# Kernel tuning notes

Measured on AMD Instinct MI355X. Metric: run time of the kernel, lower is better.

Reference implementation:

```python
import jax, jax.numpy as jnp
import numpy as np

EMBED_DIM = 512
NUM_HEADS = 8
HEAD_DIM = EMBED_DIM // NUM_HEADS


def setup_inputs() -> dict:
    key = jax.random.key(0)
    k_x, k_qkv, k_proj, k_pb = jax.random.split(key, 4)
    B, N, C = 2, 4096, EMBED_DIM
    x = jax.random.normal(k_x, (B, N, C), dtype=jnp.float32)
    # nn.Linear(embed_dim, 3*embed_dim, bias=False): weight [3C, C], y = x @ W.T
    s = 1.0 / np.sqrt(C)
    w_qkv = jax.random.uniform(k_qkv, (3 * C, C), dtype=jnp.float32, minval=-s, maxval=s)
    w_proj = jax.random.uniform(k_proj, (C, C), dtype=jnp.float32, minval=-s, maxval=s)
    b_proj = jax.random.uniform(k_pb, (C,), dtype=jnp.float32, minval=-s, maxval=s)
    return {"x": x, "w_qkv": w_qkv, "w_proj": w_proj, "b_proj": b_proj}


def reference(x, w_qkv, w_proj, b_proj):
    B, N, C = x.shape
    H, D = NUM_HEADS, HEAD_DIM
    scale = D ** -0.5
    qkv = jnp.einsum('bnc,fc->bnf', x, w_qkv)           # [B, N, 3C]
    qkv = qkv.reshape(B, N, 3, H, D)
    q, k, v = [jnp.transpose(qkv[:, :, i], (0, 2, 1, 3)) for i in range(3)]  # [B,H,N,D]
    attn = jnp.einsum('bhnd,bhmd->bhnm', q, k) * scale  # [B,H,N,N]
    # additive causal mask: -inf above the diagonal
    causal = jnp.triu(jnp.full((N, N), -jnp.inf, dtype=attn.dtype), k=1)
    attn = jax.nn.softmax(attn + causal, axis=-1)
    out = jnp.einsum('bhnm,bhmd->bhnd', attn, v)        # [B,H,N,D]
    out = jnp.transpose(out, (0, 2, 1, 3)).reshape(B, N, C)
    return jnp.einsum('bnc,oc->bno', out, w_proj) + b_proj
```

## Files before the change

### kernel.cpp

```cpp
#include <hip/hip_runtime.h>
#include <hip/hip_bf16.h>


typedef __attribute__((ext_vector_type(8))) short s16x8;
typedef __attribute__((ext_vector_type(4))) float f32x4;

#define QSCALE 0.18033688011112042f

__device__ __forceinline__ ushort f2bf(float f) {
  unsigned u = __float_as_uint(f);
  u = (u + 0x7FFFu + ((u >> 16) & 1u)) >> 16;
  return (ushort)u;
}

__device__ __forceinline__ unsigned cvt_pk_bf16(float a, float b) {
  unsigned r;
  asm("v_cvt_pk_bf16_f32 %0, %1, %2" : "=v"(r) : "v"(a), "v"(b));
  return r;
}

__device__ __forceinline__ float bflo(unsigned u) { return __uint_as_float(u << 16); }
__device__ __forceinline__ float bfhi(unsigned u) { return __uint_as_float(u & 0xffff0000u); }

__global__ __launch_bounds__(256) void cvt_all(const float* __restrict__ x,
                                               const float* __restrict__ wq,
                                               const float* __restrict__ wp,
                                               ushort* __restrict__ xb,
                                               ushort* __restrict__ wqb,
                                               ushort* __restrict__ wpb) {
  int i = blockIdx.x * 256 + threadIdx.x;
  const float* src;
  ushort* dst;
  int off;
  if (i < 1048576) {
    src = x; dst = xb; off = i;
  } else if (i < 1245184) {
    src = wq; dst = wqb; off = i - 1048576;
  } else {
    src = wp; dst = wpb; off = i - 1245184;
  }
  float4 v = reinterpret_cast<const float4*>(src)[off];
  ushort4 o;
  o.x = f2bf(v.x); o.y = f2bf(v.y); o.z = f2bf(v.z); o.w = f2bf(v.w);
  reinterpret_cast<ushort4*>(dst)[off] = o;
}

template <int EPI>
__global__ __launch_bounds__(256) void gemm_bt(const ushort* __restrict__ A,
                                               const ushort* __restrict__ W,
                                               ushort* __restrict__ q_ws,
                                               ushort* __restrict__ k_ws,
                                               ushort* __restrict__ vt_ws,
                                               float* __restrict__ outf,
                                               const float* __restrict__ bias) {
  __shared__ ushort As[2][128 * 32];
  __shared__ ushort Bs[2][128 * 32];
  const int tid = threadIdx.x;
  const int lane = tid & 63, wv = tid >> 6;
  const int wm = wv >> 1, wn = wv & 1;
  const int l15 = lane & 15, g = lane >> 4;
  const int tm = blockIdx.y * 128, tn = blockIdx.x * 128;

  f32x4 acc[4][4] = {};

#define GSTAGE(BUF, K0)                                                                    \
  do {                                                                                     \
    _Pragma("unroll") for (int it = 0; it < 2; ++it) {                                     \
      int slot = it * 256 + tid;                                                           \
      int row = slot >> 2;                                                                 \
      int ch = (slot & 3) ^ ((row >> 1) & 3);                                              \
      const int sb = (it * 256 + wv * 64) * 8;        \
      __builtin_amdgcn_global_load_lds(                                                    \
          (const __attribute__((address_space(1))) void*)(A + (size_t)(tm + row) * 512 +   \
                                                          (K0) + ch * 8),                  \
          (__attribute__((address_space(3))) void*)(&As[BUF][0] + sb), 16, 0, 0);          \
      __builtin_amdgcn_global_load_lds(                                                    \
          (const __attribute__((address_space(1))) void*)(W + (size_t)(tn + row) * 512 +   \
                                                          (K0) + ch * 8),                  \
          (__attribute__((address_space(3))) void*)(&Bs[BUF][0] + sb), 16, 0, 0);          \
    }                                                                                      \
  } while (0)

  GSTAGE(0, 0);
  __syncthreads();
  int cur = 0;
  for (int t = 0; t < 16; ++t) {
    if (t < 15) GSTAGE(cur ^ 1, (t + 1) * 32);
    s16x8 af[4], bfr[4];
#pragma unroll
    for (int i = 0; i < 4; ++i) {
      int Ra = wm * 64 + i * 16 + l15;
      af[i] = reinterpret_cast<const s16x8*>(&As[cur][0])[Ra * 4 + (g ^ ((Ra >> 1) & 3))];
      int Rb = wn * 64 + i * 16 + l15;
      bfr[i] = reinterpret_cast<const s16x8*>(&Bs[cur][0])[Rb * 4 + (g ^ ((Rb >> 1) & 3))];
    }
#pragma unroll
    for (int mi = 0; mi < 4; ++mi)
#pragma unroll
      for (int ni = 0; ni < 4; ++ni)
        acc[mi][ni] =
            __builtin_amdgcn_mfma_f32_16x16x32_bf16(af[mi], bfr[ni], acc[mi][ni], 0, 0, 0);
    __syncthreads();
    cur ^= 1;
  }
#undef GSTAGE

  const int rowb = tm + wm * 64 + g * 4;
  const int colb = tn + wn * 64 + l15;
#pragma unroll
  for (int mi = 0; mi < 4; ++mi) {
#pragma unroll
    for (int ni = 0; ni < 4; ++ni) {
      int r0 = rowb + mi * 16;
      int col = colb + ni * 16;
      if (EPI == 0) {
        int i3 = col >> 9, h = (col >> 6) & 7, d = col & 63;
        int b = r0 >> 12;
        int bh = b * 8 + h;
        if (i3 == 2) {
          int n0 = r0 & 4095;
          int kt = n0 >> 6, ce = (n0 >> 5) & 1, ge = (n0 >> 3) & 3, je = n0 & 7;
          int nbe = d >> 4, le = d & 15;
          ushort4 pk;
          pk.x = f2bf(acc[mi][ni][0]);
          pk.y = f2bf(acc[mi][ni][1]);
          pk.z = f2bf(acc[mi][ni][2]);
          pk.w = f2bf(acc[mi][ni][3]);
          *reinterpret_cast<ushort4*>(
              vt_ws + (((size_t)bh * 64 + kt) * 8 + nbe * 2 + ce) * 512 + (ge * 16 + le) * 8 +
              je) = pk;
        } else if (i3 == 1) {
          int ce = d >> 5, ge = (d >> 3) & 3, je = d & 7;
#pragma unroll
          for (int r = 0; r < 4; ++r) {
            int n = (r0 + r) & 4095;
            int kt = n >> 6, le = n & 15, nbe = (n >> 4) & 3;
            k_ws[(((size_t)bh * 64 + kt) * 8 + nbe * 2 + ce) * 512 + (ge * 16 + le) * 8 + je] =
                f2bf(acc[mi][ni][r]);
          }
        } else {
          int n0 = r0 & 4095;
#pragma unroll
          for (int r = 0; r < 4; ++r)
            q_ws[((size_t)bh * 4096 + (n0 + r)) * 64 + d] = f2bf(acc[mi][ni][r] * QSCALE);
        }
      } else {
#pragma unroll
        for (int r = 0; r < 4; ++r)
          outf[(size_t)(r0 + r) * 512 + col] = acc[mi][ni][r] + bias[col];
      }
    }
  }
}

__global__ __launch_bounds__(64, 2) void attn_kernel(const ushort* __restrict__ Q,
                                                     const ushort* __restrict__ Kk,
                                                     const ushort* __restrict__ Vt,
                                                     ushort* __restrict__ O,
                                                     ushort* __restrict__ po,
                                                     float* __restrict__ ml) {
  __shared__ ushort P_lds[32 * 64];
  const int lane = threadIdx.x & 63;
  const int l15 = lane & 15, g = lane >> 4;
  const int L = blockIdx.x;
  const int p = L & 7, j2 = L >> 3;
  const int bh = p * 2 + (j2 & 1);
  const int i = j2 >> 1;
  const int r = i / 3;
  const int kind = i - r * 3;
  int qt, klo, khi, half = 0;
  bool partial;
  if (kind == 2) {
    qt = 63 - r;
    partial = false;
    klo = 0;
    khi = qt >> 1;
  } else {
    qt = 127 - r;
    partial = true;
    half = kind;
    const int ktm = qt >> 1;
    const int mid = (ktm + 2) >> 1;
    klo = kind ? mid : 0;
    khi = kind ? ktm : (mid - 1);
  }
  const int ktmax = qt >> 1;
  const int qw = qt * 32;
  const size_t baseQ = (size_t)bh * 4096 * 64;

  s16x8 aq[2][2];
#pragma unroll
  for (int s = 0; s < 2; ++s) {
    const ushort* qp = Q + baseQ + (size_t)(qw + s * 16 + l15) * 64 + g * 8;
    aq[s][0] = *reinterpret_cast<const s16x8*>(qp);
    aq[s][1] = *reinterpret_cast<const s16x8*>(qp + 32);
  }

  f32x4 o[2][4] = {};
  float m[2] = {-1e30f, -1e30f};
  float l[2] = {0.f, 0.f};
  const int swz = (l15 & 7) << 3;
  const ushort* kb = Kk + ((size_t)bh * 64) * 4096 + lane * 8;
  const ushort* vb = Vt + ((size_t)bh * 64) * 4096 + lane * 8;

  s16x8 kfA[8], kfB[8];
#pragma unroll
  for (int t = 0; t < 8; ++t)
    kfA[t] = *reinterpret_cast<const s16x8*>(kb + (size_t)klo * 4096 + t * 512);

#define ATTN_STEP(KC, KN, KT)                                                             \
  do {                                                                                    \
    const ushort* vp = vb + (size_t)(KT) * 4096;                                          \
    s16x8 vf[8];                                                                          \
    _Pragma("unroll") for (int t = 0; t < 8; ++t)                                         \
        vf[t] = *reinterpret_cast<const s16x8*>(vp + t * 512);                            \
    const int knx = ((KT) >= khi) ? khi : ((KT) + 1);                                     \
    const ushort* kpn = kb + (size_t)knx * 4096;                                          \
    _Pragma("unroll") for (int t = 0; t < 8; ++t)                                         \
        KN[t] = *reinterpret_cast<const s16x8*>(kpn + t * 512);                           \
    f32x4 st[2][4] = {};                                                                  \
    __builtin_amdgcn_s_setprio(1);                                                        \
    _Pragma("unroll") for (int nb = 0; nb < 4; ++nb) {                                    \
      _Pragma("unroll") for (int s = 0; s < 2; ++s) {                                     \
        st[s][nb] = __builtin_amdgcn_mfma_f32_16x16x32_bf16(KC[nb * 2 + 0], aq[s][0],     \
                                                            st[s][nb], 0, 0, 0);         \
        st[s][nb] = __builtin_amdgcn_mfma_f32_16x16x32_bf16(KC[nb * 2 + 1], aq[s][1],     \
                                                            st[s][nb], 0, 0, 0);         \
      }                                                                                   \
    }                                                                                     \
    __builtin_amdgcn_s_setprio(0);                                                        \
    if ((KT) == ktmax) {                                  \
      const int k0d = (KT) * 64;                                                          \
      _Pragma("unroll") for (int s = 0; s < 2; ++s)                                       \
          _Pragma("unroll") for (int nb = 0; nb < 4; ++nb)                                \
              _Pragma("unroll") for (int r2 = 0; r2 < 4; ++r2)                            \
                  if (k0d + nb * 16 + g * 4 + r2 > qw + s * 16 + l15)                     \
                    st[s][nb][r2] = -1e30f;                                               \
    }                                                                                     \
    _Pragma("unroll") for (int s = 0; s < 2; ++s) {                                       \
      float a0 = fmaxf(fmaxf(st[s][0][0], st[s][0][1]), fmaxf(st[s][0][2], st[s][0][3])); \
      float a1 = fmaxf(fmaxf(st[s][1][0], st[s][1][1]), fmaxf(st[s][1][2], st[s][1][3])); \
      float a2 = fmaxf(fmaxf(st[s][2][0], st[s][2][1]), fmaxf(st[s][2][2], st[s][2][3])); \
      float a3 = fmaxf(fmaxf(st[s][3][0], st[s][3][1]), fmaxf(st[s][3][2], st[s][3][3])); \
      float pm = fmaxf(fmaxf(a0, a1), fmaxf(a2, a3));                 \
      if (!__all(pm - m[s] <= 8.0f)) {                   \
        float pmf = fmaxf(pm, __shfl_xor(pm, 16));                                        \
        pmf = fmaxf(pmf, __shfl_xor(pmf, 32));                                            \
        const float mn = fmaxf(m[s], pmf);                                                \
        const float al = __builtin_amdgcn_exp2f(m[s] - mn);                               \
        l[s] *= al;                                                                       \
        m[s] = mn;                                                                        \
        _Pragma("unroll") for (int nb = 0; nb < 4; ++nb)                                  \
            _Pragma("unroll") for (int r2 = 0; r2 < 4; ++r2) o[s][nb][r2] *= al;          \
      }                                                                                   \
      float rs = 0.f;                                                                     \
      _Pragma("unroll") for (int nb = 0; nb < 4; ++nb) {                                  \
        float p0 = __builtin_amdgcn_exp2f(st[s][nb][0] - m[s]);                           \
        float p1 = __builtin_amdgcn_exp2f(st[s][nb][1] - m[s]);                           \
        float p2 = __builtin_amdgcn_exp2f(st[s][nb][2] - m[s]);                           \
        float p3 = __builtin_amdgcn_exp2f(st[s][nb][3] - m[s]);                           \
        rs += (p0 + p1) + (p2 + p3);                                                      \
        uint2 w;                                                                          \
        w.x = cvt_pk_bf16(p0, p1);                                                        \
        w.y = cvt_pk_bf16(p2, p3);                                                        \
        *reinterpret_cast<uint2*>(P_lds + (s * 16 + l15) * 64 +                           \
                                  ((nb * 16 + g * 4) ^ swz)) = w;                         \
      }                                                                                   \
      l[s] += rs;                                                                         \
    }                                                                                     \
    s16x8 pa[2][2];                                                                       \
    _Pragma("unroll") for (int s = 0; s < 2; ++s)                                         \
        _Pragma("unroll") for (int c = 0; c < 2; ++c)                                     \
            pa[s][c] = *reinterpret_cast<const s16x8*>(P_lds + (s * 16 + l15) * 64 +      \
                                                       ((c * 32 + g * 8) ^ swz));         \
    __builtin_amdgcn_s_setprio(1);                                                        \
    _Pragma("unroll") for (int nb = 0; nb < 4; ++nb) {                                    \
      _Pragma("unroll") for (int s = 0; s < 2; ++s) {                                     \
        o[s][nb] = __builtin_amdgcn_mfma_f32_16x16x32_bf16(vf[nb * 2 + 0], pa[s][0],      \
                                                           o[s][nb], 0, 0, 0);            \
        o[s][nb] = __builtin_amdgcn_mfma_f32_16x16x32_bf16(vf[nb * 2 + 1], pa[s][1],      \
                                                           o[s][nb], 0, 0, 0);            \
      }                                                                                   \
    }                                                                                     \
    __builtin_amdgcn_s_setprio(0);                                                        \
  } while (0)

  int kt = klo;
  for (;;) {
    ATTN_STEP(kfA, kfB, kt);
    if (++kt > khi) break;
    ATTN_STEP(kfB, kfA, kt);
    if (++kt > khi) break;
  }
#undef ATTN_STEP

  float lr[2];
#pragma unroll
  for (int s = 0; s < 2; ++s) {
    float ls = l[s];
    ls += __shfl_xor(ls, 16);
    ls += __shfl_xor(ls, 32);
    lr[s] = ls;
  }

  if (!partial) {
    const int b = bh >> 3, h = bh & 7;
#pragma unroll
    for (int s = 0; s < 2; ++s) {
      const float linv = 1.0f / lr[s];
      const size_t rowo = (size_t)(b * 4096 + qw + s * 16 + l15) * 512 + h * 64;
#pragma unroll
      for (int nb = 0; nb < 4; ++nb) {
        uint2 pk;
        pk.x = cvt_pk_bf16(o[s][nb][0] * linv, o[s][nb][1] * linv);
        pk.y = cvt_pk_bf16(o[s][nb][2] * linv, o[s][nb][3] * linv);
        *reinterpret_cast<uint2*>(&O[rowo + nb * 16 + g * 4]) = pk;
      }
    }
  } else {
    const int t2 = (bh * 64 + (qt - 64)) * 2 + half;
#pragma unroll
    for (int s = 0; s < 2; ++s) {
      const float linv = 1.0f / lr[s];
      const int row = s * 16 + l15;
      const size_t pbase = ((size_t)t2 * 32 + row) * 64;
#pragma unroll
      for (int nb = 0; nb < 4; ++nb) {
        uint2 pk;
        pk.x = cvt_pk_bf16(o[s][nb][0] * linv, o[s][nb][1] * linv);
        pk.y = cvt_pk_bf16(o[s][nb][2] * linv, o[s][nb][3] * linv);
        *reinterpret_cast<uint2*>(po + pbase + nb * 16 + g * 4) = pk;
      }
      if (g == 0) {
        float2 v;
        v.x = m[s];
        v.y = lr[s];
        *reinterpret_cast<float2*>(ml + ((size_t)t2 * 32 + row) * 2) = v;
      }
    }
  }
}

__global__ __launch_bounds__(64) void attn_merge(const ushort* __restrict__ po,
                                                 const float* __restrict__ ml,
                                                 ushort* __restrict__ O) {
  const int L = blockIdx.x, tid = threadIdx.x;
  const int p = L & 7, q2 = L >> 3;
  const int bh = p * 2 + (q2 & 1);
  const int qt = 64 + (q2 >> 1);
  const int t = bh * 64 + (qt - 64);
  const int row = tid >> 1, dh = (tid & 1) * 32;
  const float2 ml0 = *reinterpret_cast<const float2*>(ml + ((size_t)(t * 2 + 0) * 32 + row) * 2);
  const float2 ml1 = *reinterpret_cast<const float2*>(ml + ((size_t)(t * 2 + 1) * 32 + row) * 2);
  const float ms = fmaxf(ml0.x, ml1.x);
  const float w0 = __builtin_amdgcn_exp2f(ml0.x - ms) * ml0.y;
  const float w1 = __builtin_amdgcn_exp2f(ml1.x - ms) * ml1.y;
  const float inv = 1.0f / (w0 + w1);
  const float c0 = w0 * inv, c1 = w1 * inv;
  const int b = bh >> 3, h = bh & 7;
  const size_t rowo = (size_t)(b * 4096 + qt * 32 + row) * 512 + h * 64 + dh;
  const ushort* p0 = po + ((size_t)(t * 2 + 0) * 32 + row) * 64 + dh;
  const ushort* p1 = po + ((size_t)(t * 2 + 1) * 32 + row) * 64 + dh;
#pragma unroll
  for (int j = 0; j < 4; ++j) {
    uint4 a = reinterpret_cast<const uint4*>(p0)[j];
    uint4 bb = reinterpret_cast<const uint4*>(p1)[j];
    uint4 out;
    out.x = cvt_pk_bf16(c0 * bflo(a.x) + c1 * bflo(bb.x), c0 * bfhi(a.x) + c1 * bfhi(bb.x));
    out.y = cvt_pk_bf16(c0 * bflo(a.y) + c1 * bflo(bb.y), c0 * bfhi(a.y) + c1 * bfhi(bb.y));
    out.z = cvt_pk_bf16(c0 * bflo(a.z) + c1 * bflo(bb.z), c0 * bfhi(a.z) + c1 * bfhi(bb.z));
    out.w = cvt_pk_bf16(c0 * bflo(a.w) + c1 * bflo(bb.w), c0 * bfhi(a.w) + c1 * bfhi(bb.w));
    reinterpret_cast<uint4*>(&O[rowo])[j] = out;
  }
}

extern "C" void kernel_launch(void* const* d_in, const int* in_sizes, int n_in,
                              void* d_out, int out_size, void* d_ws, size_t ws_size,
                              hipStream_t stream) {
  const float* x = (const float*)d_in[0];
  const float* w_qkv = (const float*)d_in[1];
  const float* w_proj = (const float*)d_in[2];
  const float* b_proj = (const float*)d_in[3];
  float* out = (float*)d_out;

  ushort* xb = (ushort*)d_ws;
  ushort* wqkvb = xb + (size_t)8192 * 512;
  ushort* wprojb = wqkvb + (size_t)1536 * 512;
  ushort* qws = wprojb + (size_t)512 * 512;
  ushort* kws = qws + (size_t)16 * 4096 * 64;
  ushort* vtws = kws + (size_t)16 * 4096 * 64;
  ushort* ows = vtws + (size_t)16 * 4096 * 64;

  cvt_all<<<5120, 256, 0, stream>>>(x, w_qkv, w_proj, xb, wqkvb, wprojb);

  gemm_bt<0><<<dim3(12, 64), 256, 0, stream>>>(xb, wqkvb, qws, kws, vtws, nullptr, nullptr);

  ushort* po = xb;
  float* ml = (float*)wqkvb;

  attn_kernel<<<3072, 64, 0, stream>>>(qws, kws, vtws, ows, po, ml);
  attn_merge<<<1024, 64, 0, stream>>>(po, ml, ows);

  gemm_bt<1><<<dim3(4, 64), 256, 0, stream>>>(ows, wprojb, nullptr, nullptr, nullptr, out,
                                              b_proj);
}
```

Baseline: 110.3 us.

## Split causal attention KV range into up to four partials with 4-way merge

Adds a second attention mode where query tiles are split over the key range into 1–4 partial blocks depending on how long their causal prefix is, with a new merge kernel that combines up to four partial outputs using their max and sum statistics. The aim is better load balance and more parallel work (5120 single-wave blocks instead of 3072) on the long-prefix tail tiles. The cost is more partial-output traffic and a heavier merge. The new path runs only when the workspace is large enough, with the old path kept as a fallback.

After: 111.5 us. Within noise of the previous version (+1.1%).

```diff
diff --git a/kernel.cpp b/kernel.cpp
--- a/kernel.cpp
+++ b/kernel.cpp
@@ -153,6 +153,7 @@
   }
 }
 
+template <int MODE>
 __global__ __launch_bounds__(64, 2) void attn_kernel(const ushort* __restrict__ Q,
                                                      const ushort* __restrict__ Kk,
                                                      const ushort* __restrict__ Vt,
@@ -165,24 +166,45 @@
   const int L = blockIdx.x;
   const int p = L & 7, j2 = L >> 3;
   const int bh = p * 2 + (j2 & 1);
-  const int i = j2 >> 1;
-  const int r = i / 3;
-  const int kind = i - r * 3;
-  int qt, klo, khi, half = 0;
+  int qt, klo, khi, slot = 0;
   bool partial;
-  if (kind == 2) {
-    qt = 63 - r;
-    partial = false;
-    klo = 0;
-    khi = qt >> 1;
+  if (MODE == 0) {
+    const int i = j2 >> 1;
+    const int r = i / 3;
+    const int kind = i - r * 3;
+    if (kind == 2) {
+      qt = 63 - r;
+      partial = false;
+      klo = 0;
+      khi = qt >> 1;
+    } else {
+      qt = 127 - r;
+      partial = true;
+      const int ktm = qt >> 1;
+      const int mid = (ktm + 2) >> 1;
+      klo = kind ? mid : 0;
+      khi = kind ? ktm : (mid - 1);
+      slot = (bh * 64 + (qt - 64)) * 2 + kind;
+    }
   } else {
-    qt = 127 - r;
-    partial = true;
-    half = kind;
-    const int ktm = qt >> 1;
-    const int mid = (ktm + 2) >> 1;
-    klo = kind ? mid : 0;
-    khi = kind ? ktm : (mid - 1);
+    const int i = j2 >> 1;
+    int part, S;
+    if (i < 128) {
+      qt = 127 - (i >> 2); part = i & 3; S = 4;
+    } else if (i < 224) {
+      int j = i - 128; int q3 = j / 3;
+      qt = 95 - q3; part = j - q3 * 3; S = 3;
+    } else if (i < 288) {
+      int j = i - 224;
+      qt = 63 - (j >> 1); part = j & 1; S = 2;
+    } else {
+      qt = 31 - (i - 288); part = 0; S = 1;
+    }
+    const int T = (qt >> 1) + 1;
+    klo = part * T / S;
+    khi = (part + 1) * T / S - 1;
+    partial = (S > 1);
+    if (partial) slot = (bh * 96 + (qt - 32)) * 4 + part;
   }
   const int ktmax = qt >> 1;
   const int qw = qt * 32;
@@ -318,12 +340,11 @@
       }
     }
   } else {
-    const int t2 = (bh * 64 + (qt - 64)) * 2 + half;
 #pragma unroll
     for (int s = 0; s < 2; ++s) {
       const float linv = 1.0f / lr[s];
       const int row = s * 16 + l15;
-      const size_t pbase = ((size_t)t2 * 32 + row) * 64;
+      const size_t pbase = ((size_t)slot * 32 + row) * 64;
 #pragma unroll
       for (int nb = 0; nb < 4; ++nb) {
         uint2 pk;
@@ -335,7 +356,7 @@
         float2 v;
         v.x = m[s];
         v.y = lr[s];
-        *reinterpret_cast<float2*>(ml + ((size_t)t2 * 32 + row) * 2) = v;
+        *reinterpret_cast<float2*>(ml + ((size_t)slot * 32 + row) * 2) = v;
       }
     }
   }
@@ -374,6 +395,76 @@
   }
 }
 
+__global__ __launch_bounds__(64) void attn_merge4(const ushort* __restrict__ po,
+                                                  const float* __restrict__ ml,
+                                                  ushort* __restrict__ O) {
+  const int M = blockIdx.x, tid = threadIdx.x;
+  const int p = M & 7, q2 = M >> 3;
+  const int bh = p * 2 + (q2 & 1);
+  const int ti = q2 >> 1;
+  const int qt = 32 + ti;
+  const int S = (qt >= 96) ? 4 : (qt >= 64) ? 3 : 2;
+  const int base = (bh * 96 + ti) * 4;
+  const int row = tid >> 1, dh = (tid & 1) * 32;
+  const float2 v0 = *reinterpret_cast<const float2*>(ml + ((size_t)(base + 0) * 32 + row) * 2);
+  const float2 v1 = *reinterpret_cast<const float2*>(ml + ((size_t)(base + 1) * 32 + row) * 2);
+  float2 v2 = {-1e30f, 0.f}, v3 = {-1e30f, 0.f};
+  if (S > 2) v2 = *reinterpret_cast<const float2*>(ml + ((size_t)(base + 2) * 32 + row) * 2);
+  if (S > 3) v3 = *reinterpret_cast<const float2*>(ml + ((size_t)(base + 3) * 32 + row) * 2);
+  const float ms = fmaxf(fmaxf(v0.x, v1.x), fmaxf(v2.x, v3.x));
+  float c0 = __builtin_amdgcn_exp2f(v0.x - ms) * v0.y;
+  float c1 = __builtin_amdgcn_exp2f(v1.x - ms) * v1.y;
+  float c2 = __builtin_amdgcn_exp2f(v2.x - ms) * v2.y;
+  float c3 = __builtin_amdgcn_exp2f(v3.x - ms) * v3.y;
+  const float inv = 1.0f / (((c0 + c1) + (c2 + c3)));
+  c0 *= inv; c1 *= inv; c2 *= inv; c3 *= inv;
+  const int b = bh >> 3, h = bh & 7;
+  const size_t rowo = (size_t)(b * 4096 + qt * 32 + row) * 512 + h * 64 + dh;
+  const ushort* p0 = po + ((size_t)(base + 0) * 32 + row) * 64 + dh;
+  const ushort* p1 = po + ((size_t)(base + 1) * 32 + row) * 64 + dh;
+  const ushort* p2 = po + ((size_t)(base + 2) * 32 + row) * 64 + dh;
+  const ushort* p3 = po + ((size_t)(base + 3) * 32 + row) * 64 + dh;
+#pragma unroll
+  for (int j = 0; j < 4; ++j) {
+    float acc0 = 0.f, acc1 = 0.f, acc2 = 0.f, acc3 = 0.f;
+    float acc4 = 0.f, acc5 = 0.f, acc6 = 0.f, acc7 = 0.f;
+    {
+      uint4 a = reinterpret_cast<const uint4*>(p0)[j];
+      acc0 += c0 * bflo(a.x); acc1 += c0 * bfhi(a.x);
+      acc2 += c0 * bflo(a.y); acc3 += c0 * bfhi(a.y);
+      acc4 += c0 * bflo(a.z); acc5 += c0 * bfhi(a.z);
+      acc6 += c0 * bflo(a.w); acc7 += c0 * bfhi(a.w);
+    }
+    {
+      uint4 a = reinterpret_cast<const uint4*>(p1)[j];
+      acc0 += c1 * bflo(a.x); acc1 += c1 * bfhi(a.x);
+      acc2 += c1 * bflo(a.y); acc3 += c1 * bfhi(a.y);
+      acc4 += c1 * bflo(a.z); acc5 += c1 * bfhi(a.z);
+      acc6 += c1 * bflo(a.w); acc7 += c1 * bfhi(a.w);
+    }
+    if (S > 2) {
+      uint4 a = reinterpret_cast<const uint4*>(p2)[j];
+      acc0 += c2 * bflo(a.x); acc1 += c2 * bfhi(a.x);
+      acc2 += c2 * bflo(a.y); acc3 += c2 * bfhi(a.y);
+      acc4 += c2 * bflo(a.z); acc5 += c2 * bfhi(a.z);
+      acc6 += c2 * bflo(a.w); acc7 += c2 * bfhi(a.w);
+    }
+    if (S > 3) {
+      uint4 a = reinterpret_cast<const uint4*>(p3)[j];
+      acc0 += c3 * bflo(a.x); acc1 += c3 * bfhi(a.x);
+      acc2 += c3 * bflo(a.y); acc3 += c3 * bfhi(a.y);
+      acc4 += c3 * bflo(a.z); acc5 += c3 * bfhi(a.z);
+      acc6 += c3 * bflo(a.w); acc7 += c3 * bfhi(a.w);
+    }
+    uint4 out;
+    out.x = cvt_pk_bf16(acc0, acc1);
+    out.y = cvt_pk_bf16(acc2, acc3);
+    out.z = cvt_pk_bf16(acc4, acc5);
+    out.w = cvt_pk_bf16(acc6, acc7);
+    reinterpret_cast<uint4*>(&O[rowo])[j] = out;
+  }
+}
+
 extern "C" void kernel_launch(void* const* d_in, const int* in_sizes, int n_in,
                               void* d_out, int out_size, void* d_ws, size_t ws_size,
                               hipStream_t stream) {
@@ -395,11 +486,19 @@
 
   gemm_bt<0><<<dim3(12, 64), 256, 0, stream>>>(xb, wqkvb, qws, kws, vtws, nullptr, nullptr);
 
-  ushort* po = xb;
-  float* ml = (float*)wqkvb;
-
-  attn_kernel<<<3072, 64, 0, stream>>>(qws, kws, vtws, ows, po, ml);
-  attn_merge<<<1024, 64, 0, stream>>>(po, ml, ows);
+  ushort* po4 = ows + (size_t)8192 * 512;
+  float* ml4 = (float*)(po4 + (size_t)6144 * 2048);
+  const bool big = ws_size >= (size_t)70778880;
+
+  if (big) {
+    attn_kernel<1><<<5120, 64, 0, stream>>>(qws, kws, vtws, ows, po4, ml4);
+    attn_merge4<<<1536, 64, 0, stream>>>(po4, ml4, ows);
+  } else {
+    ushort* po = xb;
+    float* ml = (float*)wqkvb;
+    attn_kernel<0><<<3072, 64, 0, stream>>>(qws, kws, vtws, ows, po, ml);
+    attn_merge<<<1024, 64, 0, stream>>>(po, ml, ows);
+  }
 
   gemm_bt<1><<<dim3(4, 64), 256, 0, stream>>>(ows, wprojb, nullptr, nullptr, nullptr, out,
                                               b_proj);
```

## Share K/V tiles in LDS across four q-tile waves with async double buffering

Applied to the files above, without the earlier changes.

The attention kernel now runs 256-thread blocks in which four waves handle four consecutive query tiles. They share K/V tiles staged into LDS through double-buffered global_load_lds, replacing per-wave direct global loads, and the launch bounds target 3 blocks per CU. The work split changes so every query tile is split into two key-range halves and always merged, and the block order is snake-permuted for load balance. This cuts redundant global K/V traffic, but it adds block-wide barriers, idle waves on tiles outside their causal range, and a larger merge pass over all query tiles.

Measured after the change: 109.1 us. No clear change (-1.1%).

```diff
diff --git a/kernel.cpp b/kernel.cpp
--- a/kernel.cpp
+++ b/kernel.cpp
@@ -153,38 +153,36 @@
   }
 }
 
-__global__ __launch_bounds__(64, 2) void attn_kernel(const ushort* __restrict__ Q,
-                                                     const ushort* __restrict__ Kk,
-                                                     const ushort* __restrict__ Vt,
-                                                     ushort* __restrict__ O,
-                                                     ushort* __restrict__ po,
-                                                     float* __restrict__ ml) {
-  __shared__ ushort P_lds[32 * 64];
-  const int lane = threadIdx.x & 63;
+__global__ __launch_bounds__(256, 3) void attn_kernel(const ushort* __restrict__ Q,
+                                                      const ushort* __restrict__ Kk,
+                                                      const ushort* __restrict__ Vt,
+                                                      ushort* __restrict__ po,
+                                                      float* __restrict__ ml) {
+  __shared__ ushort Ks[2][4096];
+  __shared__ ushort Vs[2][4096];
+  __shared__ ushort P_lds[4][32 * 64];
+  const int tid = threadIdx.x;
+  const int lane = tid & 63, wv = tid >> 6;
   const int l15 = lane & 15, g = lane >> 4;
   const int L = blockIdx.x;
-  const int p = L & 7, j2 = L >> 3;
+  const int p = L & 7;
+  int j2 = L >> 3;
+  {
+    const int pos = j2 & 31, quarter = j2 >> 5;
+    if (quarter & 1) j2 = quarter * 32 + (31 - pos);
+  }
   const int bh = p * 2 + (j2 & 1);
   const int i = j2 >> 1;
-  const int r = i / 3;
-  const int kind = i - r * 3;
-  int qt, klo, khi, half = 0;
-  bool partial;
-  if (kind == 2) {
-    qt = 63 - r;
-    partial = false;
-    klo = 0;
-    khi = qt >> 1;
-  } else {
-    qt = 127 - r;
-    partial = true;
-    half = kind;
-    const int ktm = qt >> 1;
-    const int mid = (ktm + 2) >> 1;
-    klo = kind ? mid : 0;
-    khi = kind ? ktm : (mid - 1);
-  }
+  const int G = 31 - (i >> 1);
+  const int h = i & 1;
+  const int qt = 4 * G + wv;
   const int ktmax = qt >> 1;
+  const int mid = G + 1;
+  const int klo = h ? mid : 0;
+  const int khi = h ? ktmax : (mid - 1);
+  const int KLO = h ? mid : 0;
+  const int KHI = h ? (2 * G + 1) : (mid - 1);
+  const int slot = (bh * 128 + qt) * 2 + h;
   const int qw = qt * 32;
   const size_t baseQ = (size_t)bh * 4096 * 64;
 
@@ -200,99 +198,115 @@
   float m[2] = {-1e30f, -1e30f};
   float l[2] = {0.f, 0.f};
   const int swz = (l15 & 7) << 3;
-  const ushort* kb = Kk + ((size_t)bh * 64) * 4096 + lane * 8;
-  const ushort* vb = Vt + ((size_t)bh * 64) * 4096 + lane * 8;
-
-  s16x8 kfA[8], kfB[8];
-#pragma unroll
-  for (int t = 0; t < 8; ++t)
-    kfA[t] = *reinterpret_cast<const s16x8*>(kb + (size_t)klo * 4096 + t * 512);
-
-#define ATTN_STEP(KC, KN, KT)                                                             \
+  ushort* pl = P_lds[wv];
+
+#define KVSTAGE(BUF, KT)                                                                  \
   do {                                                                                    \
-    const ushort* vp = vb + (size_t)(KT) * 4096;                                          \
-    s16x8 vf[8];                                                                          \
-    _Pragma("unroll") for (int t = 0; t < 8; ++t)                                         \
-        vf[t] = *reinterpret_cast<const s16x8*>(vp + t * 512);                            \
-    const int knx = ((KT) >= khi) ? khi : ((KT) + 1);                                     \
-    const ushort* kpn = kb + (size_t)knx * 4096;                                          \
-    _Pragma("unroll") for (int t = 0; t < 8; ++t)                                         \
-        KN[t] = *reinterpret_cast<const s16x8*>(kpn + t * 512);                           \
-    f32x4 st[2][4] = {};                                                                  \
-    __builtin_amdgcn_s_setprio(1);                                                        \
-    _Pragma("unroll") for (int nb = 0; nb < 4; ++nb) {                                    \
-      _Pragma("unroll") for (int s = 0; s < 2; ++s) {                                     \
-        st[s][nb] = __builtin_amdgcn_mfma_f32_16x16x32_bf16(KC[nb * 2 + 0], aq[s][0],     \
-                                                            st[s][nb], 0, 0, 0);         \
-        st[s][nb] = __builtin_amdgcn_mfma_f32_16x16x32_bf16(KC[nb * 2 + 1], aq[s][1],     \
-                                                            st[s][nb], 0, 0, 0);         \
-      }                                                                                   \
+    const ushort* kSrc = Kk + ((size_t)bh * 64 + (KT)) * 4096;                            \
+    const ushort* vSrc = Vt + ((size_t)bh * 64 + (KT)) * 4096;                            \
+    _Pragma("unroll") for (int c = 0; c < 2; ++c) {                                       \
+      const int sb = (c * 256 + wv * 64) * 8;        \
+      __builtin_amdgcn_global_load_lds(                                                   \
+          (const __attribute__((address_space(1))) void*)(kSrc + sb + lane * 8),          \
+          (__attribute__((address_space(3))) void*)(&Ks[BUF][0] + sb), 16, 0, 0);         \
+      __builtin_amdgcn_global_load_lds(                                                   \
+          (const __attribute__((address_space(1))) void*)(vSrc + sb + lane * 8),          \
+          (__attribute__((address_space(3))) void*)(&Vs[BUF][0] + sb), 16, 0, 0);         \
     }                                                                                     \
-    __builtin_amdgcn_s_setprio(0);                                                        \
-    if ((KT) == ktmax) {                                  \
-      const int k0d = (KT) * 64;                                                          \
-      _Pragma("unroll") for (int s = 0; s < 2; ++s)                                       \
-          _Pragma("unroll") for (int nb = 0; nb < 4; ++nb)                                \
-              _Pragma("unroll") for (int r2 = 0; r2 < 4; ++r2)                            \
-                  if (k0d + nb * 16 + g * 4 + r2 > qw + s * 16 + l15)                     \
-                    st[s][nb][r2] = -1e30f;                                               \
-    }                                                                                     \
-    _Pragma("unroll") for (int s = 0; s < 2; ++s) {                                       \
-      float a0 = fmaxf(fmaxf(st[s][0][0], st[s][0][1]), fmaxf(st[s][0][2], st[s][0][3])); \
-      float a1 = fmaxf(fmaxf(st[s][1][0], st[s][1][1]), fmaxf(st[s][1][2], st[s][1][3])); \
-      float a2 = fmaxf(fmaxf(st[s][2][0], st[s][2][1]), fmaxf(st[s][2][2], st[s][2][3])); \
-      float a3 = fmaxf(fmaxf(st[s][3][0], st[s][3][1]), fmaxf(st[s][3][2], st[s][3][3])); \
-      float pm = fmaxf(fmaxf(a0, a1), fmaxf(a2, a3));                 \
-      if (!__all(pm - m[s] <= 8.0f)) {                   \
-        float pmf = fmaxf(pm, __shfl_xor(pm, 16));                                        \
-        pmf = fmaxf(pmf, __shfl_xor(pmf, 32));                                            \
-        const float mn = fmaxf(m[s], pmf);                                                \
-        const float al = __builtin_amdgcn_exp2f(m[s] - mn);                               \
-        l[s] *= al;                                                                       \
-        m[s] = mn;                                                                        \
-        _Pragma("unroll") for (int nb = 0; nb < 4; ++nb)                                  \
-            _Pragma("unroll") for (int r2 = 0; r2 < 4; ++r2) o[s][nb][r2] *= al;          \
-      }                                                                                   \
-      float rs = 0.f;                                                                     \
-      _Pragma("unroll") for (int nb = 0; nb < 4; ++nb) {                                  \
-        float p0 = __builtin_amdgcn_exp2f(st[s][nb][0] - m[s]);                           \
-        float p1 = __builtin_amdgcn_exp2f(st[s][nb][1] - m[s]);                           \
-        float p2 = __builtin_amdgcn_exp2f(st[s][nb][2] - m[s]);                           \
-        float p3 = __builtin_amdgcn_exp2f(st[s][nb][3] - m[s]);                           \
-        rs += (p0 + p1) + (p2 + p3);                                                      \
-        uint2 w;                                                                          \
-        w.x = cvt_pk_bf16(p0, p1);                                                        \
-        w.y = cvt_pk_bf16(p2, p3);                                                        \
-        *reinterpret_cast<uint2*>(P_lds + (s * 16 + l15) * 64 +                           \
-                                  ((nb * 16 + g * 4) ^ swz)) = w;                         \
-      }                                                                                   \
-      l[s] += rs;                                                                         \
-    }                                                                                     \
-    s16x8 pa[2][2];                                                                       \
-    _Pragma("unroll") for (int s = 0; s < 2; ++s)                                         \
-        _Pragma("unroll") for (int c = 0; c < 2; ++c)                                     \
-            pa[s][c] = *reinterpret_cast<const s16x8*>(P_lds + (s * 16 + l15) * 64 +      \
-                                                       ((c * 32 + g * 8) ^ swz));         \
-    __builtin_amdgcn_s_setprio(1);                                                        \
-    _Pragma("unroll") for (int nb = 0; nb < 4; ++nb) {                                    \
-      _Pragma("unroll") for (int s = 0; s < 2; ++s) {                                     \
-        o[s][nb] = __builtin_amdgcn_mfma_f32_16x16x32_bf16(vf[nb * 2 + 0], pa[s][0],      \
-                                                           o[s][nb], 0, 0, 0);            \
-        o[s][nb] = __builtin_amdgcn_mfma_f32_16x16x32_bf16(vf[nb * 2 + 1], pa[s][1],      \
-                                                           o[s][nb], 0, 0, 0);            \
-      }                                                                                   \
-    }                                                                                     \
-    __builtin_amdgcn_s_setprio(0);                                                        \
   } while (0)
 
-  int kt = klo;
-  for (;;) {
-    ATTN_STEP(kfA, kfB, kt);
-    if (++kt > khi) break;
-    ATTN_STEP(kfB, kfA, kt);
-    if (++kt > khi) break;
-  }
-#undef ATTN_STEP
+  KVSTAGE(0, KLO);
+  __syncthreads();
+  int cur = 0;
+  for (int kt = KLO; kt <= KHI; ++kt) {
+    if (kt < KHI) KVSTAGE(cur ^ 1, kt + 1);
+    if (kt >= klo && kt <= khi) {
+      const ushort* kl = &Ks[cur][lane * 8];
+      const ushort* vl = &Vs[cur][lane * 8];
+      s16x8 kf[8], vf[8];
+#pragma unroll
+      for (int t = 0; t < 8; ++t) kf[t] = *reinterpret_cast<const s16x8*>(kl + t * 512);
+#pragma unroll
+      for (int t = 0; t < 8; ++t) vf[t] = *reinterpret_cast<const s16x8*>(vl + t * 512);
+      f32x4 st[2][4] = {};
+      __builtin_amdgcn_s_setprio(1);
+#pragma unroll
+      for (int nb = 0; nb < 4; ++nb)
+#pragma unroll
+        for (int s = 0; s < 2; ++s) {
+          st[s][nb] = __builtin_amdgcn_mfma_f32_16x16x32_bf16(kf[nb * 2 + 0], aq[s][0],
+                                                              st[s][nb], 0, 0, 0);
+          st[s][nb] = __builtin_amdgcn_mfma_f32_16x16x32_bf16(kf[nb * 2 + 1], aq[s][1],
+                                                              st[s][nb], 0, 0, 0);
+        }
+      __builtin_amdgcn_s_setprio(0);
+      if (kt == ktmax) {
+        const int k0d = kt * 64;
+#pragma unroll
+        for (int s = 0; s < 2; ++s)
+#pragma unroll
+          for (int nb = 0; nb < 4; ++nb)
+#pragma unroll
+            for (int r2 = 0; r2 < 4; ++r2)
+              if (k0d + nb * 16 + g * 4 + r2 > qw + s * 16 + l15) st[s][nb][r2] = -1e30f;
+      }
+#pragma unroll
+      for (int s = 0; s < 2; ++s) {
+        float a0 = fmaxf(fmaxf(st[s][0][0], st[s][0][1]), fmaxf(st[s][0][2], st[s][0][3]));
+        float a1 = fmaxf(fmaxf(st[s][1][0], st[s][1][1]), fmaxf(st[s][1][2], st[s][1][3]));
+        float a2 = fmaxf(fmaxf(st[s][2][0], st[s][2][1]), fmaxf(st[s][2][2], st[s][2][3]));
+        float a3 = fmaxf(fmaxf(st[s][3][0], st[s][3][1]), fmaxf(st[s][3][2], st[s][3][3]));
+        float pm = fmaxf(fmaxf(a0, a1), fmaxf(a2, a3));
+        if (!__all(pm - m[s] <= 8.0f)) {
+          float pmf = fmaxf(pm, __shfl_xor(pm, 16));
+          pmf = fmaxf(pmf, __shfl_xor(pmf, 32));
+          const float mn = fmaxf(m[s], pmf);
+          const float al = __builtin_amdgcn_exp2f(m[s] - mn);
+          l[s] *= al;
+          m[s] = mn;
+#pragma unroll
+          for (int nb = 0; nb < 4; ++nb)
+#pragma unroll
+            for (int r2 = 0; r2 < 4; ++r2) o[s][nb][r2] *= al;
+        }
+        float rs = 0.f;
+#pragma unroll
+        for (int nb = 0; nb < 4; ++nb) {
+          float p0 = __builtin_amdgcn_exp2f(st[s][nb][0] - m[s]);
+          float p1 = __builtin_amdgcn_exp2f(st[s][nb][1] - m[s]);
+          float p2 = __builtin_amdgcn_exp2f(st[s][nb][2] - m[s]);
+          float p3 = __builtin_amdgcn_exp2f(st[s][nb][3] - m[s]);
+          rs += (p0 + p1) + (p2 + p3);
+          uint2 w;
+          w.x = cvt_pk_bf16(p0, p1);
+          w.y = cvt_pk_bf16(p2, p3);
+          *reinterpret_cast<uint2*>(pl + (s * 16 + l15) * 64 + ((nb * 16 + g * 4) ^ swz)) = w;
+        }
+        l[s] += rs;
+      }
+      s16x8 pa[2][2];
+#pragma unroll
+      for (int s = 0; s < 2; ++s)
+#pragma unroll
+        for (int c = 0; c < 2; ++c)
+          pa[s][c] = *reinterpret_cast<const s16x8*>(pl + (s * 16 + l15) * 64 +
+                                                     ((c * 32 + g * 8) ^ swz));
+      __builtin_amdgcn_s_setprio(1);
+#pragma unroll
+      for (int nb = 0; nb < 4; ++nb)
+#pragma unroll
+        for (int s = 0; s < 2; ++s) {
+          o[s][nb] = __builtin_amdgcn_mfma_f32_16x16x32_bf16(vf[nb * 2 + 0], pa[s][0],
+                                                             o[s][nb], 0, 0, 0);
+          o[s][nb] = __builtin_amdgcn_mfma_f32_16x16x32_bf16(vf[nb * 2 + 1], pa[s][1],
+                                                             o[s][nb], 0, 0, 0);
+        }
+      __builtin_amdgcn_s_setprio(0);
+    }
+    __syncthreads();
+    cur ^= 1;
+  }
+#undef KVSTAGE
 
   float lr[2];
 #pragma unroll
@@ -303,40 +317,23 @@
     lr[s] = ls;
   }
 
-  if (!partial) {
-    const int b = bh >> 3, h = bh & 7;
-#pragma unroll
-    for (int s = 0; s < 2; ++s) {
-      const float linv = 1.0f / lr[s];
-      const size_t rowo = (size_t)(b * 4096 + qw + s * 16 + l15) * 512 + h * 64;
-#pragma unroll
-      for (int nb = 0; nb < 4; ++nb) {
-        uint2 pk;
-        pk.x = cvt_pk_bf16(o[s][nb][0] * linv, o[s][nb][1] * linv);
-        pk.y = cvt_pk_bf16(o[s][nb][2] * linv, o[s][nb][3] * linv);
-        *reinterpret_cast<uint2*>(&O[rowo + nb * 16 + g * 4]) = pk;
-      }
+#pragma unroll
+  for (int s = 0; s < 2; ++s) {
+    const float linv = (lr[s] > 0.f) ? (1.0f / lr[s]) : 0.f;
+    const int row = s * 16 + l15;
+    const size_t pbase = ((size_t)slot * 32 + row) * 64;
+#pragma unroll
+    for (int nb = 0; nb < 4; ++nb) {
+      uint2 pk;
+      pk.x = cvt_pk_bf16(o[s][nb][0] * linv, o[s][nb][1] * linv);
+      pk.y = cvt_pk_bf16(o[s][nb][2] * linv, o[s][nb][3] * linv);
+      *reinterpret_cast<uint2*>(po + pbase + nb * 16 + g * 4) = pk;
     }
-  } else {
-    const int t2 = (bh * 64 + (qt - 64)) * 2 + half;
-#pragma unroll
-    for (int s = 0; s < 2; ++s) {
-      const float linv = 1.0f / lr[s];
-      const int row = s * 16 + l15;
-      const size_t pbase = ((size_t)t2 * 32 + row) * 64;
-#pragma unroll
-      for (int nb = 0; nb < 4; ++nb) {
-        uint2 pk;
-        pk.x = cvt_pk_bf16(o[s][nb][0] * linv, o[s][nb][1] * linv);
-        pk.y = cvt_pk_bf16(o[s][nb][2] * linv, o[s][nb][3] * linv);
-        *reinterpret_cast<uint2*>(po + pbase + nb * 16 + g * 4) = pk;
-      }
-      if (g == 0) {
-        float2 v;
-        v.x = m[s];
-        v.y = lr[s];
-        *reinterpret_cast<float2*>(ml + ((size_t)t2 * 32 + row) * 2) = v;
-      }
+    if (g == 0) {
+      float2 v;
+      v.x = m[s];
+      v.y = lr[s];
+      *reinterpret_cast<float2*>(ml + ((size_t)slot * 32 + row) * 2) = v;
     }
   }
 }
@@ -344,11 +341,11 @@
 __global__ __launch_bounds__(64) void attn_merge(const ushort* __restrict__ po,
                                                  const float* __restrict__ ml,
                                                  ushort* __restrict__ O) {
-  const int L = blockIdx.x, tid = threadIdx.x;
-  const int p = L & 7, q2 = L >> 3;
+  const int M = blockIdx.x, tid = threadIdx.x;
+  const int p = M & 7, q2 = M >> 3;
   const int bh = p * 2 + (q2 & 1);
-  const int qt = 64 + (q2 >> 1);
-  const int t = bh * 64 + (qt - 64);
+  const int qt = q2 >> 1;
+  const int t = bh * 128 + qt;
   const int row = tid >> 1, dh = (tid & 1) * 32;
   const float2 ml0 = *reinterpret_cast<const float2*>(ml + ((size_t)(t * 2 + 0) * 32 + row) * 2);
   const float2 ml1 = *reinterpret_cast<const float2*>(ml + ((size_t)(t * 2 + 1) * 32 + row) * 2);
@@ -395,11 +392,11 @@
 
   gemm_bt<0><<<dim3(12, 64), 256, 0, stream>>>(xb, wqkvb, qws, kws, vtws, nullptr, nullptr);
 
-  ushort* po = xb;
-  float* ml = (float*)wqkvb;
-
-  attn_kernel<<<3072, 64, 0, stream>>>(qws, kws, vtws, ows, po, ml);
-  attn_merge<<<1024, 64, 0, stream>>>(po, ml, ows);
+  ushort* po = ows + (size_t)8192 * 512;
+  float* ml = (float*)(po + (size_t)2048 * 2 * 32 * 64);
+
+  attn_kernel<<<1024, 256, 0, stream>>>(qws, kws, vtws, po, ml);
+  attn_merge<<<2048, 64, 0, stream>>>(po, ml, ows);
 
   gemm_bt<1><<<dim3(4, 64), 256, 0, stream>>>(ows, wprojb, nullptr, nullptr, nullptr, out,
                                               b_proj);
```
